# Kernel tuning notes

Hardware: AMD Instinct MI355X
Metric: run time of the kernel (lower is better)

## Reference

```python
import jax, jax.numpy as jnp
import numpy as np

NUM_CLASSES = 4
E = float(np.e)


def _batched_counts(ids, num_classes):
    # ids: [B, H, W] int -> per-batch class histogram [B, num_classes] (float)
    flat = ids.reshape(ids.shape[0], -1)
    counts = jax.vmap(lambda r: jnp.bincount(r, length=num_classes))(flat)
    return counts.astype(jnp.float32)


def setup_inputs() -> dict:
    key = jax.random.key(0)
    k1, k2, k3 = jax.random.split(key, 3)
    B, C, H, W = 16, NUM_CLASSES, 768, 768
    net_output = jax.random.normal(k1, (B, C, H, W), dtype=jnp.float32)
    target = jax.random.randint(k2, (B, 1, H, W), 0, C, dtype=jnp.int32)
    bare_weight = jax.random.normal(k3, (B, C), dtype=jnp.float32)
    return {"net_output": net_output, "target": target, "bare_weight": bare_weight}


def reference(net_output, target, bare_weight):
    B, C, H, W = net_output.shape
    tgt = target[:, 0]  # squeeze channel -> [B, H, W] class indices

    # p_pred_num: per-batch histogram of argmax-predicted classes
    pred_ids = jnp.argmax(net_output, axis=1)          # [B, H, W]
    p_pred_num = _batched_counts(pred_ids, C)          # [B, C]

    # fixed weighting: argmax over target's singleton channel dim -> all zeros
    # (faithful to the torch code: batch_member.argmax(0) on [1,H,W])
    gt_ids = jnp.argmax(target, axis=1)                # [B, H, W], all zeros
    gt_num = _batched_counts(gt_ids, C)                # [B, C]
    fixed_w = jnp.log(gt_num + E) + E                  # [B, C]

    # CE kept per-class: -one_hot * log_softmax, mean over spatial dims
    one_hot = jax.nn.one_hot(tgt, C, dtype=net_output.dtype, axis=1)   # [B, C, H, W]
    dp_loss = (-one_hot * jax.nn.log_softmax(net_output, axis=1)).mean(axis=(-2, -1))  # [B, C]

    w = jax.nn.sigmoid(bare_weight)                    # [B, C]
    w = w / w.mean(axis=0)
    w = w / fixed_w

    risk_regularization = -w * p_pred_num / (H * W)    # [B, C]
    return (dp_loss * w)[:, 1:].sum() + risk_regularization[:, 1:].sum()
```

## Files before the change

### kernel.cpp

```cpp
#include <hip/hip_runtime.h>
#include <math.h>

constexpr int B = 16, C = 4, H = 768, W = 768;
constexpr int HW = H * W;
constexpr int G_PER_B = HW / 4;
constexpr int CHUNKS = 128;
constexpr int G_PER_CHUNK = G_PER_B / CHUNKS;
constexpr float LN2 = 0.6931471805599453f;
constexpr float L2E = 1.4426950408889634f;
constexpr float EULER = 2.71828182845904523536f;

__global__ __launch_bounds__(256) void dp_main_kernel(
    const float* __restrict__ net,
    const int* __restrict__ target,
    float* __restrict__ gdp,
    int* __restrict__ gcnt)
{
    const int b = blockIdx.x / CHUNKS;
    const int chunk = blockIdx.x % CHUNKS;

    const float4* __restrict__ n4 = (const float4*)(net + (size_t)b * C * HW);
    const int4* __restrict__ t4 = (const int4*)(target + (size_t)b * HW);

    float dp0 = 0.f, dp1 = 0.f, dp2 = 0.f, dp3 = 0.f;
    int c0 = 0, c1 = 0, c2 = 0, c3 = 0;

    __shared__ float sdp[C];
    __shared__ int scnt[C];
    if (threadIdx.x < C) { sdp[threadIdx.x] = 0.f; scnt[threadIdx.x] = 0; }
    __syncthreads();

    const int base = chunk * G_PER_CHUNK;
    for (int i = threadIdx.x; i < G_PER_CHUNK; i += 256) {
        const int g = base + i;
        const float4 a0 = n4[g];
        const float4 a1 = n4[g + G_PER_B];
        const float4 a2 = n4[g + 2 * G_PER_B];
        const float4 a3 = n4[g + 3 * G_PER_B];
        const int4 tv = t4[g];

        const float X0[4] = {a0.x, a0.y, a0.z, a0.w};
        const float X1[4] = {a1.x, a1.y, a1.z, a1.w};
        const float X2[4] = {a2.x, a2.y, a2.z, a2.w};
        const float X3[4] = {a3.x, a3.y, a3.z, a3.w};
        const int   T[4]  = {tv.x, tv.y, tv.z, tv.w};

#pragma unroll
        for (int j = 0; j < 4; ++j) {
            const float x0 = X0[j], x1 = X1[j], x2 = X2[j], x3 = X3[j];
            const int t = T[j];

            float m = x0; int am = 0;
            if (x1 > m) { m = x1; am = 1; }
            if (x2 > m) { m = x2; am = 2; }
            if (x3 > m) { m = x3; am = 3; }

            const float s = exp2f((x0 - m) * L2E) + exp2f((x1 - m) * L2E)
                          + exp2f((x2 - m) * L2E) + exp2f((x3 - m) * L2E);
            const float lse = m + log2f(s) * LN2;

            const float xt = (t == 0) ? x0 : (t == 1) ? x1 : (t == 2) ? x2 : x3;
            const float val = lse - xt;

            dp0 += (t == 0) ? val : 0.f;
            dp1 += (t == 1) ? val : 0.f;
            dp2 += (t == 2) ? val : 0.f;
            dp3 += (t == 3) ? val : 0.f;
            c0 += (am == 0);
            c1 += (am == 1);
            c2 += (am == 2);
            c3 += (am == 3);
        }
    }

#pragma unroll
    for (int off = 32; off > 0; off >>= 1) {
        dp0 += __shfl_down(dp0, off);
        dp1 += __shfl_down(dp1, off);
        dp2 += __shfl_down(dp2, off);
        dp3 += __shfl_down(dp3, off);
        c0 += __shfl_down(c0, off);
        c1 += __shfl_down(c1, off);
        c2 += __shfl_down(c2, off);
        c3 += __shfl_down(c3, off);
    }

    if ((threadIdx.x & 63) == 0) {
        atomicAdd(&sdp[0], dp0); atomicAdd(&sdp[1], dp1);
        atomicAdd(&sdp[2], dp2); atomicAdd(&sdp[3], dp3);
        atomicAdd(&scnt[0], c0); atomicAdd(&scnt[1], c1);
        atomicAdd(&scnt[2], c2); atomicAdd(&scnt[3], c3);
    }
    __syncthreads();

    if (threadIdx.x < C) {
        atomicAdd(&gdp[b * C + threadIdx.x], sdp[threadIdx.x]);
        atomicAdd(&gcnt[b * C + threadIdx.x], scnt[threadIdx.x]);
    }
}

__global__ __launch_bounds__(64) void dp_finalize_kernel(
    const float* __restrict__ gdp,
    const int* __restrict__ gcnt,
    const float* __restrict__ bw,
    float* __restrict__ out)
{
    const int lane = threadIdx.x;
    const int c = lane & 3;

    const float s = 1.0f / (1.0f + expf(-bw[lane]));

    float colsum = s;
#pragma unroll
    for (int off = 4; off < 64; off <<= 1) colsum += __shfl_xor(colsum, off);
    const float colmean = colsum * (1.0f / (float)B);

    const float fixed_w = (c == 0) ? (logf((float)HW + EULER) + EULER)
                                   : (1.0f + EULER);
    const float w = s / colmean / fixed_w;

    float term = 0.f;
    if (c >= 1) {
        term = w * (gdp[lane] - (float)gcnt[lane]) * (1.0f / (float)HW);
    }
#pragma unroll
    for (int off = 1; off < 64; off <<= 1) term += __shfl_xor(term, off);

    if (lane == 0) out[0] = term;
}

extern "C" void kernel_launch(void* const* d_in, const int* in_sizes, int n_in,
                              void* d_out, int out_size, void* d_ws, size_t ws_size,
                              hipStream_t stream) {
    const float* net = (const float*)d_in[0];
    const int* target = (const int*)d_in[1];
    const float* bw = (const float*)d_in[2];
    float* out = (float*)d_out;

    float* gdp = (float*)d_ws;
    int* gcnt = (int*)((char*)d_ws + B * C * sizeof(float));

    hipMemsetAsync(d_ws, 0, B * C * (sizeof(float) + sizeof(int)), stream);

    dp_main_kernel<<<B * CHUNKS, 256, 0, stream>>>(net, target, gdp, gcnt);
    dp_finalize_kernel<<<1, 64, 0, stream>>>(gdp, gcnt, bw, out);
}
```

Baseline: 245.7 us.

## Replace atomics and memset with per-wave partial slots reduced in finalize

Each wave now writes its partial class sums and argmax counts to a dedicated slot instead of doing shared and global atomics. This removes the workspace memset launch and the block synchronisation. The finalize kernel now sums the slots. The chunk count is retuned so every thread runs a fixed number of iterations with unrolling. The trade-off is extra serial reduction work in the single-wave finalize kernel.

```diff
diff --git a/kernel.cpp b/kernel.cpp
--- a/kernel.cpp
+++ b/kernel.cpp
@@ -4,8 +4,11 @@
 constexpr int B = 16, C = 4, H = 768, W = 768;
 constexpr int HW = H * W;
 constexpr int G_PER_B = HW / 4;
-constexpr int CHUNKS = 128;
+constexpr int CHUNKS = 96;
 constexpr int G_PER_CHUNK = G_PER_B / CHUNKS;
+constexpr int ITERS = G_PER_CHUNK / 256;
+constexpr int WAVES = 4;
+constexpr int SLOTS = CHUNKS * WAVES;
 constexpr float LN2 = 0.6931471805599453f;
 constexpr float L2E = 1.4426950408889634f;
 constexpr float EULER = 2.71828182845904523536f;
@@ -13,8 +16,8 @@
 __global__ __launch_bounds__(256) void dp_main_kernel(
     const float* __restrict__ net,
     const int* __restrict__ target,
-    float* __restrict__ gdp,
-    int* __restrict__ gcnt)
+    float* __restrict__ pdp,
+    float* __restrict__ pcnt)
 {
     const int b = blockIdx.x / CHUNKS;
     const int chunk = blockIdx.x % CHUNKS;
@@ -25,14 +28,10 @@
     float dp0 = 0.f, dp1 = 0.f, dp2 = 0.f, dp3 = 0.f;
     int c0 = 0, c1 = 0, c2 = 0, c3 = 0;
 
-    __shared__ float sdp[C];
-    __shared__ int scnt[C];
-    if (threadIdx.x < C) { sdp[threadIdx.x] = 0.f; scnt[threadIdx.x] = 0; }
-    __syncthreads();
-
-    const int base = chunk * G_PER_CHUNK;
-    for (int i = threadIdx.x; i < G_PER_CHUNK; i += 256) {
-        const int g = base + i;
+    const int base = chunk * G_PER_CHUNK + threadIdx.x;
+#pragma unroll 2
+    for (int k = 0; k < ITERS; ++k) {
+        const int g = base + k * 256;
         const float4 a0 = n4[g];
         const float4 a1 = n4[g + G_PER_B];
         const float4 a2 = n4[g + 2 * G_PER_B];
@@ -85,28 +84,40 @@
         c3 += __shfl_down(c3, off);
     }
 
-    if ((threadIdx.x & 63) == 0) {
-        atomicAdd(&sdp[0], dp0); atomicAdd(&sdp[1], dp1);
-        atomicAdd(&sdp[2], dp2); atomicAdd(&sdp[3], dp3);
-        atomicAdd(&scnt[0], c0); atomicAdd(&scnt[1], c1);
-        atomicAdd(&scnt[2], c2); atomicAdd(&scnt[3], c3);
-    }
-    __syncthreads();
-
-    if (threadIdx.x < C) {
-        atomicAdd(&gdp[b * C + threadIdx.x], sdp[threadIdx.x]);
-        atomicAdd(&gcnt[b * C + threadIdx.x], scnt[threadIdx.x]);
+    const int lane = threadIdx.x & 63;
+    const int wid = threadIdx.x >> 6;
+    if (lane == 0) {
+        const int s0 = (b * C) * SLOTS + chunk * WAVES + wid;
+        pdp[s0]             = dp0;
+        pdp[s0 + SLOTS]     = dp1;
+        pdp[s0 + 2 * SLOTS] = dp2;
+        pdp[s0 + 3 * SLOTS] = dp3;
+        pcnt[s0]             = (float)c0;
+        pcnt[s0 + SLOTS]     = (float)c1;
+        pcnt[s0 + 2 * SLOTS] = (float)c2;
+        pcnt[s0 + 3 * SLOTS] = (float)c3;
     }
 }
 
 __global__ __launch_bounds__(64) void dp_finalize_kernel(
-    const float* __restrict__ gdp,
-    const int* __restrict__ gcnt,
+    const float* __restrict__ pdp,
+    const float* __restrict__ pcnt,
     const float* __restrict__ bw,
     float* __restrict__ out)
 {
     const int lane = threadIdx.x;
     const int c = lane & 3;
+
+    const float4* __restrict__ dp4 = (const float4*)(pdp + lane * SLOTS);
+    const float4* __restrict__ ct4 = (const float4*)(pcnt + lane * SLOTS);
+    float dp = 0.f, cnt = 0.f;
+#pragma unroll 4
+    for (int k = 0; k < SLOTS / 4; ++k) {
+        const float4 a = dp4[k];
+        const float4 d = ct4[k];
+        dp += (a.x + a.y) + (a.z + a.w);
+        cnt += (d.x + d.y) + (d.z + d.w);
+    }
 
     const float s = 1.0f / (1.0f + expf(-bw[lane]));
 
@@ -121,7 +132,7 @@
 
     float term = 0.f;
     if (c >= 1) {
-        term = w * (gdp[lane] - (float)gcnt[lane]) * (1.0f / (float)HW);
+        term = w * (dp - cnt) * (1.0f / (float)HW);
     }
 #pragma unroll
     for (int off = 1; off < 64; off <<= 1) term += __shfl_xor(term, off);
@@ -137,11 +148,9 @@
     const float* bw = (const float*)d_in[2];
     float* out = (float*)d_out;
 
-    float* gdp = (float*)d_ws;
-    int* gcnt = (int*)((char*)d_ws + B * C * sizeof(float));
+    float* pdp = (float*)d_ws;
+    float* pcnt = (float*)((char*)d_ws + B * C * SLOTS * sizeof(float));
 
-    hipMemsetAsync(d_ws, 0, B * C * (sizeof(float) + sizeof(int)), stream);
-
-    dp_main_kernel<<<B * CHUNKS, 256, 0, stream>>>(net, target, gdp, gcnt);
-    dp_finalize_kernel<<<1, 64, 0, stream>>>(gdp, gcnt, bw, out);
+    dp_main_kernel<<<B * CHUNKS, 256, 0, stream>>>(net, target, pdp, pcnt);
+    dp_finalize_kernel<<<1, 64, 0, stream>>>(pdp, pcnt, bw, out);
 }
```

After: 249.5 us. Within noise of the previous version (+1.5%).
